# Optimization experiments

Hardware: AMD Instinct MI355X
Metric: run time of the kernel (lower is better)

## Reference

```python
import jax
jax.config.update('jax_enable_x64', True)  # exact int64 phase products (torch builds phasors in complex128)
import jax.numpy as jnp
import numpy as np

L = 393216          # seq_length, divisible by Locc=4, K=12, mmse_block=12
K = 12              # ktc=4 -> K=12
LOCC = 4            # _compute_locc for ktc=4
U, P = 8, 4         # max_users, max_ports_per_user
BLK = 12            # mmse_block_size
SEARCH_MIN, SEARCH_MAX = -10, 10


def setup_inputs() -> dict:
    key = jax.random.key(0)
    k1, k2, k3 = jax.random.split(key, 3)
    ls_real = jax.random.normal(k1, (L,), dtype=jnp.float32)
    ls_imag = jax.random.normal(k2, (L,), dtype=jnp.float32)
    cyclic_shifts = jax.random.randint(k3, (U, P), 0, K)  # int, values in [0, K)
    return {"ls_real": ls_real, "ls_imag": ls_imag, "cyclic_shifts": cyclic_shifts}


def _phasor(m):
    """exp(1j*2*pi*m*n/L) for each m in the [UP] vector -> [UP, L] complex64.
    Phase reduced mod L in exact int64 before float conversion for accuracy."""
    n = jnp.arange(L, dtype=jnp.int64)
    r = (m.astype(jnp.int64)[:, None] * n[None, :]) % L      # exact
    ang = (2.0 * np.pi / L) * r.astype(jnp.float32)
    return jnp.exp(1j * ang).astype(jnp.complex64)


def _forward(ls, cyclic_shifts):
    shifts = cyclic_shifts.reshape(-1)                        # [UP]
    ideal_peak = ((K - shifts) % K) * L // K                  # [UP]

    # --- timing offset search in +/-10 window around ideal peak (CIR domain) ---
    h_time = jnp.fft.ifft(ls)                                 # IDFT
    h_mag = jnp.abs(h_time) ** 2                              # [L]
    offs = jnp.arange(SEARCH_MIN, SEARCH_MAX + 1)             # [21]
    win = (ideal_peak[:, None] + offs[None, :]) % L           # [UP, 21]
    T = offs[jnp.argmax(h_mag[win], axis=1)]                  # [UP] timing offsets
    m = T + ideal_peak                                        # [UP]

    ph_m = _phasor(m)                                         # [UP, L]
    ph_T = _phasor(T)                                         # [UP, L]

    # --- per-port cyclic de-shift, OCC demux (avg of 4), linear interp back to L ---
    h_up = ls[None, :] * ph_m                                 # [UP, L]
    h_avg = h_up.reshape(-1, L // LOCC, LOCC).mean(-1)        # [UP, L/4]
    orig_idx = (LOCC - 1) / 2.0 + LOCC * jnp.arange(L // LOCC, dtype=jnp.float32)
    new_idx = jnp.arange(L, dtype=jnp.float32)
    interp1 = jax.vmap(lambda y: jnp.interp(new_idx, orig_idx, y))
    h_interp = (interp1(h_avg.real.astype(jnp.float32))
                + 1j * interp1(h_avg.imag.astype(jnp.float32))).astype(jnp.complex64)  # [UP, L]

    # --- residual reconstruction and re-addition per port ---
    h_recon = jnp.sum(h_interp * jnp.conj(ph_m), axis=0)      # [L]
    residual = ls - h_recon
    h_wr = h_interp + residual[None, :] * ph_m                # [UP, L]

    # --- noise power estimate from adjacent-sample differences ---
    diff = ls[1:] - ls[:-1]
    noise_power = jnp.mean(jnp.abs(diff) ** 2) / 2

    # --- block MMSE: h_mmse = C (C + R)^-1 h with default C = I, R = sigma^2 I ---
    C = jnp.eye(BLK, dtype=jnp.complex64)
    Rm = noise_power.astype(jnp.complex64) * jnp.eye(BLK, dtype=jnp.complex64)
    M = C @ jnp.linalg.inv(C + Rm)                            # [12, 12]
    hb = h_wr.reshape(-1, L // BLK, BLK)                      # [UP, L/12, 12]
    h_mmse = jnp.einsum('ij,ubj->ubi', M, hb).reshape(-1, L)  # [UP, L]

    # --- align back by conj timing phasor ---
    return h_mmse * jnp.conj(ph_T)                            # [UP, L] complex64


def reference(ls_real, ls_imag, cyclic_shifts):
    ls = (ls_real + 1j * ls_imag).astype(jnp.complex64)
    return _forward(ls, cyclic_shifts)
```

## Files before the change

kernel.cpp:

```cpp
#include <hip/hip_runtime.h>
#include <math.h>

#define L_TOT 393216
#define L_D4  98304
#define NPORT 32
#define NPEAK 12
#define NOFF  21
#define NCAND 252
#define TILE  1536
#define NBLK  (L_TOT / TILE)
#define NSLOT 12
#define HALF_ELEMS 12582912ull

__device__ float2 g_F[NBLK * NCAND];
__device__ double g_npart[NBLK];
__device__ int    g_prm[96];
__device__ float  g_scale[1];
__device__ int    g_ticket = 0;

__constant__ double c_cos12[12] = {1.0, 0.8660254037844387, 0.5, 0.0, -0.5,
  -0.8660254037844387, -1.0, -0.8660254037844387, -0.5, 0.0, 0.5, 0.8660254037844387};
__constant__ double c_sin12[12] = {0.0, 0.5, 0.8660254037844387, 1.0,
  0.8660254037844387, 0.5, 0.0, -0.5, -0.8660254037844387, -1.0,
  -0.8660254037844387, -0.5};

__device__ __forceinline__ void interp_coords(int n, int* j0, float* f) {
  float x = ((float)n - 1.5f) * 0.25f;
  if (x <= 0.f)                    { *j0 = 0;        *f = 0.f; }
  else if (x >= (float)(L_D4 - 1)) { *j0 = L_D4 - 2; *f = 1.f; }
  else { int jj = (int)x; *j0 = jj; *f = x - (float)jj; }
}

__device__ __forceinline__ float2 zpowS(float2 z, float2 z2, float2 z4, float2 z8, int T) {
  int t = T < 0 ? -T : T;
  float cr = 1.f, ci = 0.f;
  if (t & 1) { cr = z.x; ci = z.y; }
  if (t & 2) { float a = cr*z2.x - ci*z2.y, b = cr*z2.y + ci*z2.x; cr = a; ci = b; }
  if (t & 4) { float a = cr*z4.x - ci*z4.y, b = cr*z4.y + ci*z4.x; cr = a; ci = b; }
  if (t & 8) { float a = cr*z8.x - ci*z8.y, b = cr*z8.y + ci*z8.x; cr = a; ci = b; }
  if (T < 0) ci = -ci;
  return make_float2(cr, ci);
}

__global__ __launch_bounds__(256) void search_kernel(
    const float* __restrict__ lsr, const float* __restrict__ lsi,
    const int* __restrict__ shifts) {
  __shared__ float2 sh_ls[TILE + 1];
  __shared__ float2 sh_z[TILE];
  __shared__ float2 sh_red[NCAND * NOFF];
  __shared__ bool   sh_last;
  const float w = (float)(2.0 * M_PI / (double)L_TOT);
  int tid = threadIdx.x;
  int KB = blockIdx.x * TILE;
  for (int i = tid; i < TILE + 1; i += 256) {
    int k = KB + i; if (k > L_TOT - 1) k = L_TOT - 1;
    sh_ls[i] = make_float2(lsr[k], lsi[k]);
  }
  for (int i = tid; i < TILE; i += 256) {
    float s, c; __sincosf(w * (float)(KB + i), &s, &c);
    sh_z[i] = make_float2(c, s);
  }
  __syncthreads();

  if (tid < NCAND) {
    int r = tid % 12, lane = tid / 12;
    float accr[NOFF], acci[NOFF];
#pragma unroll
    for (int d = 0; d < NOFF; ++d) { accr[d] = 0.f; acci[d] = 0.f; }
    for (int q = lane; q < TILE / 12; q += 21) {
      int kl = 12 * q + r;
      float2 y = sh_ls[kl];
      float2 z = sh_z[kl];
      accr[10] += y.x; acci[10] += y.y;
      float cpr = y.x, cpi = y.y, cmr = y.x, cmi = y.y;
#pragma unroll
      for (int d = 1; d <= 10; ++d) {
        float tr = cpr*z.x - cpi*z.y, ti = cpr*z.y + cpi*z.x; cpr = tr; cpi = ti;
        accr[10 + d] += cpr; acci[10 + d] += cpi;
        tr = cmr*z.x + cmi*z.y; ti = cmi*z.x - cmr*z.y; cmr = tr; cmi = ti;
        accr[10 - d] += cmr; acci[10 - d] += cmi;
      }
    }
#pragma unroll
    for (int d = 0; d < NOFF; ++d)
      sh_red[tid * NOFF + d] = make_float2(accr[d], acci[d]);
  }
  double nacc = 0.0;
  int top = (KB + TILE <= L_TOT - 1) ? TILE : (L_TOT - 1 - KB);
  for (int i = tid; i < top; i += 256) {
    float2 a = sh_ls[i], b = sh_ls[i + 1];
    float dr = b.x - a.x, di = b.y - a.y;
    nacc += (double)(dr * dr + di * di);
  }
  __syncthreads();
  if (tid < NCAND) {
    int r = tid / NOFF, dd = tid - r * NOFF;
    float fr = 0.f, fi = 0.f;
    for (int lane = 0; lane < 21; ++lane) {
      float2 v = sh_red[(lane * 12 + r) * NOFF + dd];
      fr += v.x; fi += v.y;
    }
    g_F[blockIdx.x * NCAND + tid] = make_float2(fr, fi);
  }
  __syncthreads();
  double* nb = (double*)sh_red;
  nb[tid] = nacc;
  __syncthreads();
  for (int t = 128; t > 0; t >>= 1) {
    if (tid < t) nb[tid] += nb[tid + t];
    __syncthreads();
  }
  if (tid == 0) g_npart[blockIdx.x] = nb[0];

  __syncthreads();
  if (tid == 0) {
    __threadfence();
    int old = atomicAdd(&g_ticket, 1);
    sh_last = (old == NBLK - 1);
  }
  __syncthreads();
  if (!sh_last) return;
  __threadfence();

  double* db  = (double*)sh_red;
  double* sGr = db;
  double* sGi = db + 252;
  double* hm  = db + 504;
  double* nrd = db + 756;
  int* pu = (int*)(db + 1024);
  int* Tu = pu + 32;

  if (tid < NCAND) {
    double gr = 0.0, gi = 0.0;
    for (int b = 0; b < NBLK; ++b) {
      float2 v = g_F[b * NCAND + tid];
      gr += (double)v.x; gi += (double)v.y;
    }
    sGr[tid] = gr; sGi[tid] = gi;
  }
  nrd[tid] = g_npart[tid];
  __syncthreads();
  if (tid < NCAND) {
    int p = tid / NOFF, dd = tid - p * NOFF;
    double sr = 0.0, si = 0.0;
    for (int r = 0; r < 12; ++r) {
      int idx = (p * r) % 12;
      double gr = sGr[r * NOFF + dd], gi = sGi[r * NOFF + dd];
      sr += c_cos12[idx] * gr - c_sin12[idx] * gi;
      si += c_cos12[idx] * gi + c_sin12[idx] * gr;
    }
    hm[tid] = sr * sr + si * si;
  }
  __syncthreads();
  for (int t = 128; t > 0; t >>= 1) {
    if (tid < t) nrd[tid] += nrd[tid + t];
    __syncthreads();
  }
  if (tid < NPORT) {
    int s = shifts[tid];
    int p = (NPEAK - (s % NPEAK)) % NPEAK;
    double best = -1.0; int bd = 0;
    for (int d = 0; d < NOFF; ++d) {
      double v = hm[p * NOFF + d];
      if (v > best) { best = v; bd = d; }
    }
    pu[tid] = p;
    Tu[tid] = bd - 10;
  }
  __syncthreads();
  if (tid == 0) {
    int nd = 0;
    int pv[NSLOT], tv[NSLOT], mv[NSLOT], cv[NSLOT]; unsigned msk[NSLOT];
#pragma unroll
    for (int s = 0; s < NSLOT; ++s) { pv[s] = 0; tv[s] = 0; mv[s] = 0; cv[s] = 0; msk[s] = 0u; }
    for (int u = 0; u < NPORT; ++u) {
      int p = pu[u];
      int slot = -1;
      for (int s = 0; s < nd; ++s) if (pv[s] == p) { slot = s; break; }
      if (slot < 0) {
        slot = nd++;
        pv[slot] = p; tv[slot] = Tu[u];
        int m = Tu[u] + p * (L_TOT / NPEAK);
        if (m < 0) m += L_TOT;
        mv[slot] = m;
      }
      cv[slot] += 1;
      msk[slot] |= (1u << u);
    }
    g_prm[0] = nd;
#pragma unroll
    for (int s = 0; s < NSLOT; ++s) {
      g_prm[1 + s]  = pv[s];
      g_prm[13 + s] = tv[s];
      g_prm[25 + s] = mv[s];
      g_prm[37 + s] = cv[s];
      g_prm[49 + s] = (int)msk[s];
    }
    double npow = nrd[0] / (double)(L_TOT - 1) * 0.5;
    g_scale[0] = (float)(1.0 / (1.0 + npow));
    __threadfence();
    atomicExch(&g_ticket, 0);
  }
}

__global__ __launch_bounds__(256) void fused_kernel(
    const float* __restrict__ lsr, const float* __restrict__ lsi,
    float* __restrict__ out, unsigned long long out_elems) {
  __shared__ float2 sh_ls[264];
  __shared__ float2 sh_h[16][67];
  __shared__ float2 sh_tbl[144];
  __shared__ float2 sh_stp1[NSLOT];
  __shared__ int    sm_T[NSLOT], sm_p[NSLOT], sm_m[NSLOT], sm_cnt[NSLOT], sm_msk[NSLOT];
  __shared__ int    sm_nd;
  __shared__ float  sm_scale;

  const float w = (float)(2.0 * M_PI / (double)L_TOT);
  int tid = threadIdx.x;
  int N0 = blockIdx.x * 256;
  int JBASE; float fd;
  interp_coords(N0, &JBASE, &fd);
  int K0 = 4 * JBASE;

  if (tid < NSLOT) {
    sm_T[tid] = g_prm[13 + tid];
    sm_p[tid] = g_prm[1 + tid];
    int m = g_prm[25 + tid]; sm_m[tid] = m;
    sm_cnt[tid] = g_prm[37 + tid];
    sm_msk[tid] = g_prm[49 + tid];
    float s, c; __sincosf(w * (float)m, &s, &c);
    sh_stp1[tid] = make_float2(c, s);
  }
  if (tid == 0) { sm_nd = g_prm[0]; sm_scale = g_scale[0]; }
  if (tid < 144) {
    int p = tid / 12, r = tid - p * 12;
    int idx = (p * r) % 12;
    float s, c; __sincosf((float)(2.0 * M_PI / 12.0) * (float)idx, &s, &c);
    sh_tbl[tid] = make_float2(c, s);
  }
  for (int i = tid; i < 264; i += 256) {
    int k = K0 + i; if (k > L_TOT - 1) k = L_TOT - 1;
    sh_ls[i] = make_float2(lsr[k], lsi[k]);
  }
  __syncthreads();

  int nd = __builtin_amdgcn_readfirstlane(sm_nd);

  for (int e = tid; e < 66 * 16; e += 256) {
    int s = e & 15, jj = e >> 4;
    if (s < nd) {
      int j = JBASE + jj; if (j > L_D4 - 1) j = L_D4 - 1;
      int k0 = 4 * j, kk = k0 - K0;
      unsigned rr = (unsigned)(((long long)sm_m[s] * k0) % L_TOT);
      float phs, phc; __sincosf(w * (float)rr, &phs, &phc);
      float2 stp = sh_stp1[s];
      float sr = 0.f, si = 0.f;
#pragma unroll
      for (int t = 0; t < 4; ++t) {
        float2 v = sh_ls[kk + t];
        sr += v.x * phc - v.y * phs;
        si += v.x * phs + v.y * phc;
        float a = phc * stp.x - phs * stp.y, b = phc * stp.y + phs * stp.x;
        phc = a; phs = b;
      }
      sh_h[s][jj] = make_float2(0.25f * sr, 0.25f * si);
    }
  }
  __syncthreads();

  int n = N0 + tid;
  int j0; float f;
  interp_coords(n, &j0, &f);
  int jj0 = j0 - JBASE;
  int r12 = n % 12;
  float2 lsn = sh_ls[n - K0];
  float zs, zc; __sincosf(w * (float)n, &zs, &zc);
  float2 zn = make_float2(zc, zs);
  float2 z2 = make_float2(zn.x*zn.x - zn.y*zn.y, 2.f*zn.x*zn.y);
  float2 z4 = make_float2(z2.x*z2.x - z2.y*z2.y, 2.f*z2.x*z2.y);
  float2 z8 = make_float2(z4.x*z4.x - z4.y*z4.y, 2.f*z4.x*z4.y);

  float aAr[NSLOT], aAi[NSLOT];
  float rcr = 0.f, rci = 0.f;
#pragma unroll
  for (int s = 0; s < NSLOT; ++s) {
    if (s < nd) {
      int T = __builtin_amdgcn_readfirstlane(sm_T[s]);
      int p = __builtin_amdgcn_readfirstlane(sm_p[s]);
      float cnt = (float)__builtin_amdgcn_readfirstlane(sm_cnt[s]);
      float2 zT = zpowS(zn, z2, z4, z8, T);
      float2 tb = sh_tbl[p * 12 + r12];
      float2 y0 = sh_h[s][jj0], y1 = sh_h[s][jj0 + 1];
      float hr = y0.x + f * (y1.x - y0.x);
      float hi = y0.y + f * (y1.y - y0.y);
      float Ar = hr * zT.x + hi * zT.y;
      float Ai = hi * zT.x - hr * zT.y;
      aAr[s] = Ar; aAi[s] = Ai;
      rcr += cnt * (Ar * tb.x + Ai * tb.y);
      rci += cnt * (Ai * tb.x - Ar * tb.y);
    } else { aAr[s] = 0.f; aAi[s] = 0.f; }
  }
  float resr = lsn.x - rcr, resi = lsn.y - rci;
  float scl = sm_scale;

  bool full = (out_elems >= 2ull * HALF_ELEMS);
#pragma unroll
  for (int s = 0; s < NSLOT; ++s) {
    if (s < nd) {
      int p = __builtin_amdgcn_readfirstlane(sm_p[s]);
      unsigned mask = (unsigned)__builtin_amdgcn_readfirstlane(sm_msk[s]);
      float2 tb = sh_tbl[p * 12 + r12];
      float orr = scl * (aAr[s] + resr * tb.x - resi * tb.y);
      float oii = scl * (aAi[s] + resr * tb.y + resi * tb.x);
      while (mask) {
        int u = __builtin_ctz(mask); mask &= mask - 1;
        unsigned long long o = (unsigned long long)u * L_TOT + (unsigned)n;
        if (full) {
          out[o] = orr;
          out[HALF_ELEMS + o] = oii;
        } else {
          if (o < out_elems)              out[o] = orr;
          if (HALF_ELEMS + o < out_elems) out[HALF_ELEMS + o] = oii;
        }
      }
    }
  }
}

extern "C" void kernel_launch(void* const* d_in, const int* in_sizes, int n_in,
                              void* d_out, int out_size, void* d_ws, size_t ws_size,
                              hipStream_t stream) {
  const float* lsr    = (const float*)d_in[0];
  const float* lsi    = (const float*)d_in[1];
  const int*   shifts = (const int*)d_in[2];
  float* out = (float*)d_out;

  if (in_sizes[0] != L_TOT || in_sizes[1] != L_TOT) return;

  unsigned long long out_elems = (unsigned long long)(out_size > 0 ? out_size : 0);

  search_kernel<<<NBLK, 256, 0, stream>>>(lsr, lsi, shifts);
  fused_kernel<<<L_TOT / 256, 256, 0, stream>>>(lsr, lsi, out, out_elems);
}
```

Measured before the change: 125.6 us.

## Stage per-slot outputs in shared memory and write float4-vectorized per-port rows

After: 123.6 us. About the same (-1.6%).

```diff
diff --git a/kernel.cpp b/kernel.cpp
--- a/kernel.cpp
+++ b/kernel.cpp
@@ -171,6 +171,7 @@
   if (tid == 0) {
     int nd = 0;
     int pv[NSLOT], tv[NSLOT], mv[NSLOT], cv[NSLOT]; unsigned msk[NSLOT];
+    int ps[NPORT];
 #pragma unroll
     for (int s = 0; s < NSLOT; ++s) { pv[s] = 0; tv[s] = 0; mv[s] = 0; cv[s] = 0; msk[s] = 0u; }
     for (int u = 0; u < NPORT; ++u) {
@@ -186,6 +187,7 @@
       }
       cv[slot] += 1;
       msk[slot] |= (1u << u);
+      ps[u] = slot;
     }
     g_prm[0] = nd;
 #pragma unroll
@@ -196,6 +198,7 @@
       g_prm[37 + s] = cv[s];
       g_prm[49 + s] = (int)msk[s];
     }
+    for (int u = 0; u < NPORT; ++u) g_prm[61 + u] = ps[u];
     double npow = nrd[0] / (double)(L_TOT - 1) * 0.5;
     g_scale[0] = (float)(1.0 / (1.0 + npow));
     __threadfence();
@@ -206,11 +209,16 @@
 __global__ __launch_bounds__(256) void fused_kernel(
     const float* __restrict__ lsr, const float* __restrict__ lsi,
     float* __restrict__ out, unsigned long long out_elems) {
-  __shared__ float2 sh_ls[264];
-  __shared__ float2 sh_h[16][67];
+  __shared__ __align__(16) char u_mem[24576];
+  float2* sh_ls = (float2*)u_mem;
+  float2 (*sh_h)[67] = (float2 (*)[67])(u_mem + 2112);
+  float (*Rre)[256] = (float (*)[256])u_mem;
+  float (*Rim)[256] = (float (*)[256])(u_mem + 12288);
+
   __shared__ float2 sh_tbl[144];
   __shared__ float2 sh_stp1[NSLOT];
-  __shared__ int    sm_T[NSLOT], sm_p[NSLOT], sm_m[NSLOT], sm_cnt[NSLOT], sm_msk[NSLOT];
+  __shared__ int    sm_T[NSLOT], sm_p[NSLOT], sm_m[NSLOT], sm_cnt[NSLOT];
+  __shared__ int    sm_ps[NPORT];
   __shared__ int    sm_nd;
   __shared__ float  sm_scale;
 
@@ -226,10 +234,10 @@
     sm_p[tid] = g_prm[1 + tid];
     int m = g_prm[25 + tid]; sm_m[tid] = m;
     sm_cnt[tid] = g_prm[37 + tid];
-    sm_msk[tid] = g_prm[49 + tid];
     float s, c; __sincosf(w * (float)m, &s, &c);
     sh_stp1[tid] = make_float2(c, s);
   }
+  if (tid < NPORT) sm_ps[tid] = g_prm[61 + tid];
   if (tid == 0) { sm_nd = g_prm[0]; sm_scale = g_scale[0]; }
   if (tid < 144) {
     int p = tid / 12, r = tid - p * 12;
@@ -245,24 +253,29 @@
 
   int nd = __builtin_amdgcn_readfirstlane(sm_nd);
 
-  for (int e = tid; e < 66 * 16; e += 256) {
-    int s = e & 15, jj = e >> 4;
-    if (s < nd) {
-      int j = JBASE + jj; if (j > L_D4 - 1) j = L_D4 - 1;
+  {
+    int s = tid >> 4, l = tid & 15;
+    int jst = l * 5;
+    if (s < nd && jst < 66) {
+      int cnt = 66 - jst; if (cnt > 5) cnt = 5;
+      int j = JBASE + jst; if (j > L_D4 - 1) j = L_D4 - 1;
       int k0 = 4 * j, kk = k0 - K0;
       unsigned rr = (unsigned)(((long long)sm_m[s] * k0) % L_TOT);
       float phs, phc; __sincosf(w * (float)rr, &phs, &phc);
       float2 stp = sh_stp1[s];
-      float sr = 0.f, si = 0.f;
-#pragma unroll
-      for (int t = 0; t < 4; ++t) {
-        float2 v = sh_ls[kk + t];
-        sr += v.x * phc - v.y * phs;
-        si += v.x * phs + v.y * phc;
-        float a = phc * stp.x - phs * stp.y, b = phc * stp.y + phs * stp.x;
-        phc = a; phs = b;
+      for (int q = 0; q < cnt; ++q) {
+        float sr = 0.f, si = 0.f;
+#pragma unroll
+        for (int t = 0; t < 4; ++t) {
+          float2 v = sh_ls[kk + t];
+          sr += v.x * phc - v.y * phs;
+          si += v.x * phs + v.y * phc;
+          float a = phc * stp.x - phs * stp.y, b = phc * stp.y + phs * stp.x;
+          phc = a; phs = b;
+        }
+        sh_h[s][jst + q] = make_float2(0.25f * sr, 0.25f * si);
+        kk += 4;
       }
-      sh_h[s][jj] = make_float2(0.25f * sr, 0.25f * si);
     }
   }
   __syncthreads();
@@ -301,26 +314,40 @@
   }
   float resr = lsn.x - rcr, resi = lsn.y - rci;
   float scl = sm_scale;
-
-  bool full = (out_elems >= 2ull * HALF_ELEMS);
+  __syncthreads();
+
 #pragma unroll
   for (int s = 0; s < NSLOT; ++s) {
     if (s < nd) {
       int p = __builtin_amdgcn_readfirstlane(sm_p[s]);
-      unsigned mask = (unsigned)__builtin_amdgcn_readfirstlane(sm_msk[s]);
       float2 tb = sh_tbl[p * 12 + r12];
-      float orr = scl * (aAr[s] + resr * tb.x - resi * tb.y);
-      float oii = scl * (aAi[s] + resr * tb.y + resi * tb.x);
-      while (mask) {
-        int u = __builtin_ctz(mask); mask &= mask - 1;
-        unsigned long long o = (unsigned long long)u * L_TOT + (unsigned)n;
-        if (full) {
-          out[o] = orr;
-          out[HALF_ELEMS + o] = oii;
-        } else {
-          if (o < out_elems)              out[o] = orr;
-          if (HALF_ELEMS + o < out_elems) out[HALF_ELEMS + o] = oii;
-        }
+      Rre[s][tid] = scl * (aAr[s] + resr * tb.x - resi * tb.y);
+      Rim[s][tid] = scl * (aAi[s] + resr * tb.y + resi * tb.x);
+    }
+  }
+  __syncthreads();
+
+  bool full = (out_elems >= 2ull * HALF_ELEMS);
+#pragma unroll
+  for (int i = 0; i < 16; ++i) {
+    int id = tid + 256 * i;
+    int u  = id >> 7;
+    int pl = (id >> 6) & 1;
+    int c  = id & 63;
+    int s  = sm_ps[u];
+    const float* Rrow = pl ? Rim[s] : Rre[s];
+    float4 v = *(const float4*)&Rrow[4 * c];
+    unsigned long long o = (unsigned long long)u * L_TOT + (unsigned)(N0 + 4 * c)
+                         + (pl ? HALF_ELEMS : 0ull);
+    if (full) {
+      *(float4*)&out[o] = v;
+    } else {
+      if (o + 3 < out_elems) { *(float4*)&out[o] = v; }
+      else {
+        if (o < out_elems)     out[o] = v.x;
+        if (o + 1 < out_elems) out[o + 1] = v.y;
+        if (o + 2 < out_elems) out[o + 2] = v.z;
+        if (o + 3 < out_elems) out[o + 3] = v.w;
       }
     }
   }
```
